# Kernel optimization log

Measured on AMD Instinct MI355X. Metric: run time of the kernel, lower is better.

The kernel has to match this reference:

```python
import jax, jax.numpy as jnp
import numpy as np

B, N, C, O = 1, 8192, 256, 64


def setup_inputs() -> dict:
    key = jax.random.key(0)
    ks = jax.random.split(key, 7)
    return {
        "x": jax.random.normal(ks[0], (B, N, C), dtype=jnp.float32),
        "W1": jax.random.normal(ks[1], (O, C), dtype=jnp.float32) * 0.05,
        "b1": jax.random.normal(ks[2], (O,), dtype=jnp.float32) * 0.05,
        "a1": jax.random.normal(ks[3], (O,), dtype=jnp.float32) * 0.05,
        "ba1": jax.random.normal(ks[4], (1,), dtype=jnp.float32) * 0.05,
        "a2": jax.random.normal(ks[5], (O,), dtype=jnp.float32) * 0.05,
        "ba2": jax.random.normal(ks[6], (1,), dtype=jnp.float32) * 0.05,
    }


def reference(x, W1, b1, a1, ba1, a2, ba2):
    # conv1 (1x1 Conv1d) == per-node linear: seq_fts [B, O, N]
    seq_fts = jnp.einsum('bnc,oc->bon', x, W1) + b1[None, :, None]
    # conv2_1 / conv2_2 (O -> 1, 1x1): f1, f2 [B, N]
    f1 = jnp.einsum('bon,o->bn', seq_fts, a1) + ba1
    f2 = jnp.einsum('bon,o->bn', seq_fts, a2) + ba2
    # logits[b,i,j] = f1[b,i] + f2[b,j]  -> [B, N, N]
    logits = jax.nn.leaky_relu(f1[:, :, None] + f2[:, None, :], negative_slope=0.01)
    # NOTE: original uses nn.Softmax(dim=1) on [B, N, N] -> normalize over axis 1
    coefs = jax.nn.softmax(logits, axis=1)
    # ret[b,i,o] = sum_j coefs[b,i,j] * seq_fts[b,o,j]  -> [B, N, O]
    ret = jnp.einsum('bij,boj->bio', coefs, seq_fts)
    return jax.nn.elu(ret)
```

## Files before the change

### kernel.cpp

```cpp
#include <hip/hip_runtime.h>
#include <math.h>

#define NN 8192
#define CC 256
#define OO 64
#define JW 8

__global__ __launch_bounds__(256) void k_gemm(
    const float* __restrict__ x, const float* __restrict__ W1,
    const float* __restrict__ b1, const float* __restrict__ a1,
    const float* __restrict__ ba1, const float* __restrict__ a2,
    const float* __restrict__ ba2,
    float* __restrict__ seq,
    float* __restrict__ f1, float* __restrict__ f2,
    float* __restrict__ E1, float* __restrict__ E1s,
    float* __restrict__ eF2, float* __restrict__ eF2s,
    unsigned long long* __restrict__ keys )
{
  __shared__ float w_lds[64][66];
  __shared__ float x_lds[8][256];
  const int t = threadIdx.x;
  const int p = t & 31;
  const int row = t >> 5;
  const int r = blockIdx.x*8 + row;
  for (int q = t; q < 512; q += 256) {
    const int rr = q >> 6, c4 = q & 63;
    ((float4*)x_lds[rr])[c4] = ((const float4*)(x + (size_t)(blockIdx.x*8 + rr)*CC))[c4];
  }
  float c0 = 0.f, c1 = 0.f;
  for (int ct = 0; ct < 4; ++ct) {
    __syncthreads();
    for (int idx = t; idx < 4096; idx += 256) {
      const int o = idx >> 6, cc = idx & 63;
      w_lds[cc][o] = W1[o*CC + ct*64 + cc];
    }
    __syncthreads();
    const float* xr = &x_lds[row][ct*64];
#pragma unroll 4
    for (int c = 0; c < 64; c += 4) {
      const float4 xa = *(const float4*)(xr + c);
      const float2 w0 = *(const float2*)&w_lds[c+0][2*p];
      const float2 w1 = *(const float2*)&w_lds[c+1][2*p];
      const float2 w2 = *(const float2*)&w_lds[c+2][2*p];
      const float2 w3 = *(const float2*)&w_lds[c+3][2*p];
      c0 = fmaf(xa.x, w0.x, c0); c0 = fmaf(xa.y, w1.x, c0);
      c0 = fmaf(xa.z, w2.x, c0); c0 = fmaf(xa.w, w3.x, c0);
      c1 = fmaf(xa.x, w0.y, c1); c1 = fmaf(xa.y, w1.y, c1);
      c1 = fmaf(xa.z, w2.y, c1); c1 = fmaf(xa.w, w3.y, c1);
    }
  }
  const float2 B2 = *(const float2*)&b1[2*p];
  const float v0 = c0 + B2.x, v1 = c1 + B2.y;
  *(float2*)&seq[(size_t)r*OO + 2*p] = make_float2(v0, v1);
  const float2 A1 = *(const float2*)&a1[2*p];
  const float2 A2 = *(const float2*)&a2[2*p];
  float p1 = v0*A1.x + v1*A1.y;
  float p2 = v0*A2.x + v1*A2.y;
#pragma unroll
  for (int d = 1; d < 32; d <<= 1) {
    p1 += __shfl_xor(p1, d, 64);
    p2 += __shfl_xor(p2, d, 64);
  }
  if (p == 0) {
    const float t1 = p1 + ba1[0], t2 = p2 + ba2[0];
    f1[r] = t1; E1[r] = expf(t1); E1s[r] = expf(0.01f*t1);
    f2[r] = t2; eF2[r] = expf(t2); eF2s[r] = expf(0.01f*t2);
    unsigned u;
    u = __float_as_uint(t1); u = (u & 0x80000000u) ? ~u : (u | 0x80000000u);
    keys[r] = ((unsigned long long)u << 32) | (unsigned)r;
    u = __float_as_uint(t2); u = (u & 0x80000000u) ? ~u : (u | 0x80000000u);
    keys[NN + r] = ((unsigned long long)u << 32) | (unsigned)r;
  }
}

__global__ __launch_bounds__(512) void k_rank(
    const unsigned long long* __restrict__ keys,
    const float* __restrict__ f1, const float* __restrict__ E1,
    const float* __restrict__ E1s, const float* __restrict__ f2,
    const float* __restrict__ eF2, const float* __restrict__ eF2s,
    float* __restrict__ s1, float* __restrict__ se1, float* __restrict__ se1s,
    int* __restrict__ inv1,
    float* __restrict__ f2s, float* __restrict__ eF2srt,
    float* __restrict__ eF2ssrt, int* __restrict__ inv)
{
  __shared__ unsigned long long skl[NN];
  const int t = threadIdx.x;
  const int lane = t & 63, wv = t >> 6;
  const int b = blockIdx.x;
  const int arr = b >> 7;
  const int jbw = (b & 127)*64 + wv*JW;
  const unsigned long long* kb = keys + ((size_t)arr << 13);
  for (int q = t; q < NN/2; q += 512)
    ((ulonglong2*)skl)[q] = ((const ulonglong2*)kb)[q];
  __syncthreads();
  unsigned long long K[JW];
#pragma unroll
  for (int q = 0; q < JW; ++q) {
    const unsigned long long kk = skl[jbw + q];
    const unsigned lo = __builtin_amdgcn_readfirstlane((unsigned)kk);
    const unsigned hi = __builtin_amdgcn_readfirstlane((unsigned)(kk >> 32));
    K[q] = ((unsigned long long)hi << 32) | lo;
  }
  int cnt[JW];
#pragma unroll
  for (int q = 0; q < JW; ++q) cnt[q] = 0;
  const ulonglong2* s2 = (const ulonglong2*)skl;
#pragma unroll 2
  for (int c = 0; c < NN/128; ++c) {
    const ulonglong2 sk = s2[c*64 + lane];
#pragma unroll
    for (int q = 0; q < JW; ++q) {
      cnt[q] += (sk.x < K[q]) ? 1 : 0;
      cnt[q] += (sk.y < K[q]) ? 1 : 0;
    }
  }
#pragma unroll
  for (int q = 0; q < JW; ++q) {
    int r = cnt[q];
#pragma unroll
    for (int d = 1; d < 64; d <<= 1) r += __shfl_xor(r, d, 64);
    if (lane == 0) {
      const int i = jbw + q;
      if (arr == 0) {
        s1[r] = f1[i]; se1[r] = E1[i]; se1s[r] = E1s[i]; inv1[r] = i;
      } else {
        inv[r] = i; f2s[r] = f2[i]; eF2srt[r] = eF2[i]; eF2ssrt[r] = eF2s[i];
      }
    }
  }
}

__global__ __launch_bounds__(1024) void k_DT(
    const float* __restrict__ se1, const float* __restrict__ se1s,
    const float* __restrict__ s1g,
    const float* __restrict__ f2s, const float* __restrict__ eF2srt,
    const float* __restrict__ eF2ssrt, const int* __restrict__ inv,
    const float* __restrict__ seq,
    float* __restrict__ Bs, float* __restrict__ Es,
    int* __restrict__ kpos, float* __restrict__ TU, float* __restrict__ TV)
{
  __shared__ float s1l[NN];
  __shared__ float f2sl[NN];
  __shared__ float csA[256], csB[256];
  __shared__ float csEA[257], csEB[257];
  __shared__ float wsA[4], wsB[4];
  __shared__ float bsl[32], esl[32];
  __shared__ float redU[16][64], redV[16][64];
  const int t = threadIdx.x;
  const int b = blockIdx.x;
  const int wv = t >> 6, lane = t & 63;
  const float4 a0 = ((const float4*)se1 )[t*2];
  const float4 a1v = ((const float4*)se1 )[t*2+1];
  const float4 b0 = ((const float4*)se1s)[t*2];
  const float4 b1v = ((const float4*)se1s)[t*2+1];
  ((float4*)s1l)[t*2]   = ((const float4*)s1g)[t*2];
  ((float4*)s1l)[t*2+1] = ((const float4*)s1g)[t*2+1];
  ((float4*)f2sl)[t*2]   = ((const float4*)f2s)[t*2];
  ((float4*)f2sl)[t*2+1] = ((const float4*)f2s)[t*2+1];
  float sa = ((a0.x+a0.y)+(a0.z+a0.w)) + ((a1v.x+a1v.y)+(a1v.z+a1v.w));
  float sb = ((b0.x+b0.y)+(b0.z+b0.w)) + ((b1v.x+b1v.y)+(b1v.z+b1v.w));
  sa += __shfl_xor(sa, 1, 64); sb += __shfl_xor(sb, 1, 64);
  sa += __shfl_xor(sa, 2, 64); sb += __shfl_xor(sb, 2, 64);
  if ((t & 3) == 0) { csA[t>>2] = sa; csB[t>>2] = sb; }
  __syncthreads();
  if (t < 256) {
    float a = csA[t], bv = csB[t];
#pragma unroll
    for (int d = 1; d < 64; d <<= 1) {
      const float ua = __shfl_up(a, d, 64);
      const float ub = __shfl_up(bv, d, 64);
      if (lane >= d) { a += ua; bv += ub; }
    }
    csA[t] = a; csB[t] = bv;
    if (lane == 63) { wsA[wv] = a; wsB[wv] = bv; }
  }
  __syncthreads();
  if (t < 256) {
    float baseA = 0.f, baseB = 0.f;
    for (int q = 0; q < wv; ++q) { baseA += wsA[q]; baseB += wsB[q]; }
    csEA[t+1] = csA[t] + baseA;
    csEB[t+1] = csB[t] + baseB;
    if (t == 0) { csEA[0] = 0.f; csEB[0] = 0.f; }
  }
  __syncthreads();
  const int half = lane >> 5, m = lane & 31;
  {
    const int kk = b*32 + 2*wv + half;
    const float tgt = -f2sl[kk];
    int pos = 0;
#pragma unroll
    for (int s = NN; s; s >>= 1) {
      const int c = pos + s;
      if (c <= NN && s1l[c-1] < tgt) pos = c;
    }
    const int base = pos & ~31, cn = pos & 31;
    float ta = 0.f, tb = 0.f;
    if (m < cn) { ta = se1[base+m]; tb = se1s[base+m]; }
#pragma unroll
    for (int d = 1; d < 32; d <<= 1) {
      ta += __shfl_xor(ta, d, 64);
      tb += __shfl_xor(tb, d, 64);
    }
    if (m == 0) {
      const float PreA = csEA[pos>>5] + ta;
      const float PreB = csEB[pos>>5] + tb;
      const float T1 = csEA[256];
      const float e2 = eF2srt[kk], e2s = eF2ssrt[kk];
      const float D = fmaf(T1 - PreA, e2, PreB * e2s);
      const float bsv = e2 / D, esv = e2s / D;
      Bs[kk] = bsv; Es[kk] = esv;
      bsl[2*wv + half] = bsv; esl[2*wv + half] = esv;
    }
  }
  if (t < 32) {
    const int r = b*32 + t;
    const float tgt = -s1l[r];
    int pos = 0;
#pragma unroll
    for (int s = NN; s; s >>= 1) {
      const int c = pos + s;
      if (c <= NN && f2sl[c-1] < tgt) pos = c;
    }
    kpos[r] = pos;
  }
  __syncthreads();
  {
    const int kk0 = b*32 + 2*wv, kk1 = kk0 + 1;
    const float s0v = seq[(size_t)inv[kk0]*OO + lane];
    const float s1v = seq[(size_t)inv[kk1]*OO + lane];
    redU[wv][lane] = bsl[2*wv]*s0v + bsl[2*wv+1]*s1v;
    redV[wv][lane] = esl[2*wv]*s0v + esl[2*wv+1]*s1v;
  }
  __syncthreads();
  if (wv == 0) {
    float r = 0.f;
#pragma unroll
    for (int q = 0; q < 16; ++q) r += redU[q][lane];
    TU[b*64 + lane] = r;
  } else if (wv == 1) {
    float r = 0.f;
#pragma unroll
    for (int q = 0; q < 16; ++q) r += redV[q][lane];
    TV[b*64 + lane] = r;
  }
}

__global__ __launch_bounds__(1024) void k_merge(
    const int* __restrict__ kpos, const int* __restrict__ inv,
    const int* __restrict__ inv1,
    const float* __restrict__ se1, const float* __restrict__ se1s,
    const float* __restrict__ Bs, const float* __restrict__ Es,
    const float* __restrict__ seq,
    const float* __restrict__ TU, const float* __restrict__ TV,
    float* __restrict__ out)
{
  __shared__ int kposl[NN];
  __shared__ float pu[33][64], pv[33][64];
  __shared__ float rA[16][64], rB[16][64], rC[16][64];
  __shared__ int bnd[2];
  const int t = threadIdx.x, lane = t & 63, wv = t >> 6, b = blockIdx.x;
  for (int q = t; q < NN/4; q += 1024)
    ((int4*)kposl)[q] = ((const int4*)kpos)[q];
  float pbu = 0.f, pbv = 0.f, ptu = 0.f;
  for (int c = wv; c < 256; c += 16) {
    const float tu = TU[c*64 + lane], tv = TV[c*64 + lane];
    ptu += tu;
    if (c < b) { pbu += tu; pbv += tv; }
  }
  rA[wv][lane] = pbu; rB[wv][lane] = pbv; rC[wv][lane] = ptu;
  {
    const int kk0 = b*32 + 2*wv, kk1 = kk0 + 1;
    const float sv0 = seq[(size_t)inv[kk0]*OO + lane];
    const float sv1 = seq[(size_t)inv[kk1]*OO + lane];
    pu[2*wv+1][lane] = Bs[kk0]*sv0; pv[2*wv+1][lane] = Es[kk0]*sv0;
    pu[2*wv+2][lane] = Bs[kk1]*sv1; pv[2*wv+2][lane] = Es[kk1]*sv1;
  }
  if (wv == 0) { pu[0][lane] = 0.f; pv[0][lane] = 0.f; }
  __syncthreads();
  if (t == 0) {
    const int hi = 32*b + 32 + (b == 255 ? 1 : 0);
    int pos = 0;
    for (int s = NN; s; s >>= 1) { const int c = pos+s; if (c <= NN && kposl[c-1] >= hi) pos = c; }
    bnd[0] = pos;
    pos = 0;
    const int lo = 32*b;
    for (int s = NN; s; s >>= 1) { const int c = pos+s; if (c <= NN && kposl[c-1] >= lo) pos = c; }
    bnd[1] = pos;
  }
  float base_u = 0.f, base_v = 0.f, utot = 0.f;
#pragma unroll
  for (int q = 0; q < 16; ++q) {
    base_u += rA[q][lane]; base_v += rB[q][lane]; utot += rC[q][lane];
  }
  for (int d = 1; d < 32; d <<= 1) {
    const int rowA = wv + 1;
    const int rowB = wv + 17;
    const int srcA = rowA - d, srcB = rowB - d;
    const float aA = (srcA >= 0) ? pu[srcA][lane] : 0.f;
    const float vA = (srcA >= 0) ? pv[srcA][lane] : 0.f;
    const float aB = (srcB >= 0) ? pu[srcB][lane] : 0.f;
    const float vB = (srcB >= 0) ? pv[srcB][lane] : 0.f;
    __syncthreads();
    pu[rowA][lane] += aA; pv[rowA][lane] += vA;
    pu[rowB][lane] += aB; pv[rowB][lane] += vB;
    __syncthreads();
  }
  const int r0 = bnd[0], r1 = bnd[1];
  for (int r = r0 + wv; r < r1; r += 16) {
    const int kl = kposl[r] - 32*b;
    const float ret = se1[r]*(utot - (base_u + pu[kl][lane]))
                    + se1s[r]*(base_v + pv[kl][lane]);
    out[(size_t)inv1[r]*OO + lane] = (ret > 0.f) ? ret : expm1f(ret);
  }
}

extern "C" void kernel_launch(void* const* d_in, const int* in_sizes, int n_in,
                              void* d_out, int out_size, void* d_ws, size_t ws_size,
                              hipStream_t stream)
{
  (void)in_sizes; (void)n_in; (void)out_size; (void)ws_size;
  const float* x   = (const float*)d_in[0];
  const float* W1  = (const float*)d_in[1];
  const float* b1  = (const float*)d_in[2];
  const float* a1  = (const float*)d_in[3];
  const float* ba1 = (const float*)d_in[4];
  const float* a2  = (const float*)d_in[5];
  const float* ba2 = (const float*)d_in[6];
  float* out = (float*)d_out;

  float* w = (float*)d_ws;
  size_t off = 0;
  auto alloc = [&](size_t n) { float* p = w + off; off += (n + 63) & ~(size_t)63; return p; };
  float* seq  = alloc((size_t)NN*OO);
  float* f1   = alloc(NN);
  float* f2   = alloc(NN);
  float* E1   = alloc(NN);
  float* E1s  = alloc(NN);
  float* eF2  = alloc(NN);
  float* eF2s = alloc(NN);
  unsigned long long* keys = (unsigned long long*)alloc((size_t)4*NN);
  int*   inv1 = (int*)alloc(NN);
  int*   inv  = (int*)alloc(NN);
  float* s1   = alloc(NN);
  float* se1  = alloc(NN);
  float* se1s = alloc(NN);
  float* f2s  = alloc(NN);
  float* eF2srt  = alloc(NN);
  float* eF2ssrt = alloc(NN);
  float* Bs   = alloc(NN);
  float* Es   = alloc(NN);
  int*   kpos = (int*)alloc(NN);
  float* TU   = alloc(256*64);
  float* TV   = alloc(256*64);

  k_gemm<<<1024, 256, 0, stream>>>(x, W1, b1, a1, ba1, a2, ba2,
                                   seq, f1, f2, E1, E1s, eF2, eF2s, keys);
  k_rank<<<256, 512, 0, stream>>>(keys, f1, E1, E1s, f2, eF2, eF2s,
                                  s1, se1, se1s, inv1, f2s, eF2srt, eF2ssrt, inv);
  k_DT<<<256, 1024, 0, stream>>>(se1, se1s, s1, f2s, eF2srt, eF2ssrt,
                                 inv, seq, Bs, Es, kpos, TU, TV);
  k_merge<<<256, 1024, 0, stream>>>(kpos, inv, inv1, se1, se1s, Bs, Es,
                                    seq, TU, TV, out);
}
```

Before: 54.78 us.

## Compute x·W1 projection with split-bf16 MFMA instead of FP32 FMAs

Rewrites the first GEMM kernel to split x and W1 into bf16 high/low parts and accumulate three MFMA 16x16x32 products, which approximates FP32 accuracy. Each block now handles 16 rows, with one wave per 16 output columns, and W1 is read directly from global memory instead of being staged in LDS. f1/f2 are reduced from an LDS copy of the output tile. This targets the scalar FMA cost of the projection but adds split overhead and drops the low×low term, which costs a little precision.

```diff
diff --git a/kernel.cpp b/kernel.cpp
--- a/kernel.cpp
+++ b/kernel.cpp
@@ -5,6 +5,18 @@
 #define CC 256
 #define OO 64
 #define JW 8
+
+using short8 = __attribute__((ext_vector_type(8))) short;
+using f32x4  = __attribute__((ext_vector_type(4))) float;
+
+__device__ __forceinline__ void split2(const float a, const float b,
+                                       unsigned& hp, unsigned& lp) {
+  const unsigned ua = __float_as_uint(a), ub = __float_as_uint(b);
+  hp = (ua >> 16) | (ub & 0xffff0000u);
+  const float la = a - __uint_as_float(ua & 0xffff0000u);
+  const float lb = b - __uint_as_float(ub & 0xffff0000u);
+  lp = (__float_as_uint(la) >> 16) | (__float_as_uint(lb) & 0xffff0000u);
+}
 
 __global__ __launch_bounds__(256) void k_gemm(
     const float* __restrict__ x, const float* __restrict__ W1,
@@ -17,59 +29,87 @@
     float* __restrict__ eF2, float* __restrict__ eF2s,
     unsigned long long* __restrict__ keys )
 {
-  __shared__ float w_lds[64][66];
-  __shared__ float x_lds[8][256];
+  __shared__ unsigned short xh[16][264];
+  __shared__ unsigned short xl[16][264];
+  __shared__ float seq_l[16][66];
   const int t = threadIdx.x;
-  const int p = t & 31;
-  const int row = t >> 5;
-  const int r = blockIdx.x*8 + row;
-  for (int q = t; q < 512; q += 256) {
-    const int rr = q >> 6, c4 = q & 63;
-    ((float4*)x_lds[rr])[c4] = ((const float4*)(x + (size_t)(blockIdx.x*8 + rr)*CC))[c4];
-  }
-  float c0 = 0.f, c1 = 0.f;
-  for (int ct = 0; ct < 4; ++ct) {
-    __syncthreads();
-    for (int idx = t; idx < 4096; idx += 256) {
-      const int o = idx >> 6, cc = idx & 63;
-      w_lds[cc][o] = W1[o*CC + ct*64 + cc];
-    }
-    __syncthreads();
-    const float* xr = &x_lds[row][ct*64];
-#pragma unroll 4
-    for (int c = 0; c < 64; c += 4) {
-      const float4 xa = *(const float4*)(xr + c);
-      const float2 w0 = *(const float2*)&w_lds[c+0][2*p];
-      const float2 w1 = *(const float2*)&w_lds[c+1][2*p];
-      const float2 w2 = *(const float2*)&w_lds[c+2][2*p];
-      const float2 w3 = *(const float2*)&w_lds[c+3][2*p];
-      c0 = fmaf(xa.x, w0.x, c0); c0 = fmaf(xa.y, w1.x, c0);
-      c0 = fmaf(xa.z, w2.x, c0); c0 = fmaf(xa.w, w3.x, c0);
-      c1 = fmaf(xa.x, w0.y, c1); c1 = fmaf(xa.y, w1.y, c1);
-      c1 = fmaf(xa.z, w2.y, c1); c1 = fmaf(xa.w, w3.y, c1);
-    }
-  }
-  const float2 B2 = *(const float2*)&b1[2*p];
-  const float v0 = c0 + B2.x, v1 = c1 + B2.y;
-  *(float2*)&seq[(size_t)r*OO + 2*p] = make_float2(v0, v1);
-  const float2 A1 = *(const float2*)&a1[2*p];
-  const float2 A2 = *(const float2*)&a2[2*p];
-  float p1 = v0*A1.x + v1*A1.y;
-  float p2 = v0*A2.x + v1*A2.y;
-#pragma unroll
-  for (int d = 1; d < 32; d <<= 1) {
-    p1 += __shfl_xor(p1, d, 64);
-    p2 += __shfl_xor(p2, d, 64);
-  }
-  if (p == 0) {
-    const float t1 = p1 + ba1[0], t2 = p2 + ba2[0];
-    f1[r] = t1; E1[r] = expf(t1); E1s[r] = expf(0.01f*t1);
-    f2[r] = t2; eF2[r] = expf(t2); eF2s[r] = expf(0.01f*t2);
-    unsigned u;
-    u = __float_as_uint(t1); u = (u & 0x80000000u) ? ~u : (u | 0x80000000u);
-    keys[r] = ((unsigned long long)u << 32) | (unsigned)r;
-    u = __float_as_uint(t2); u = (u & 0x80000000u) ? ~u : (u | 0x80000000u);
-    keys[NN + r] = ((unsigned long long)u << 32) | (unsigned)r;
+  const int lane = t & 63, wv = t >> 6;
+  const int r0 = blockIdx.x * 16;
+  for (int q = t; q < 1024; q += 256) {
+    const int row = q >> 6, c4 = (q & 63) * 4;
+    const float4 v = *(const float4*)(x + (size_t)(r0 + row)*CC + c4);
+    unsigned hp0, lp0, hp1, lp1;
+    split2(v.x, v.y, hp0, lp0);
+    split2(v.z, v.w, hp1, lp1);
+    const int di = (row*264 + c4) >> 1;
+    ((unsigned*)xh)[di]   = hp0; ((unsigned*)xh)[di+1] = hp1;
+    ((unsigned*)xl)[di]   = lp0; ((unsigned*)xl)[di+1] = lp1;
+  }
+  __syncthreads();
+  const int lr = lane & 15;
+  const int ls = lane >> 4;
+  const int o0 = wv * 16;
+  const float* wrow = W1 + (size_t)(o0 + lr)*CC;
+  const unsigned short* xhr = &xh[lr][0];
+  const unsigned short* xlr = &xl[lr][0];
+  f32x4 acc = {0.f, 0.f, 0.f, 0.f};
+#pragma unroll
+  for (int kc = 0; kc < CC; kc += 32) {
+    const int ko = kc + ls*8;
+    const short8 a_hi = *(const short8*)(xhr + ko);
+    const short8 a_lo = *(const short8*)(xlr + ko);
+    const float4 w0 = *(const float4*)(wrow + ko);
+    const float4 w1 = *(const float4*)(wrow + ko + 4);
+    unsigned bh0, bl0, bh1, bl1, bh2, bl2, bh3, bl3;
+    split2(w0.x, w0.y, bh0, bl0);
+    split2(w0.z, w0.w, bh1, bl1);
+    split2(w1.x, w1.y, bh2, bl2);
+    split2(w1.z, w1.w, bh3, bl3);
+    short8 b_hi, b_lo;
+    b_hi[0] = (short)(bh0 & 0xffff); b_hi[1] = (short)(bh0 >> 16);
+    b_hi[2] = (short)(bh1 & 0xffff); b_hi[3] = (short)(bh1 >> 16);
+    b_hi[4] = (short)(bh2 & 0xffff); b_hi[5] = (short)(bh2 >> 16);
+    b_hi[6] = (short)(bh3 & 0xffff); b_hi[7] = (short)(bh3 >> 16);
+    b_lo[0] = (short)(bl0 & 0xffff); b_lo[1] = (short)(bl0 >> 16);
+    b_lo[2] = (short)(bl1 & 0xffff); b_lo[3] = (short)(bl1 >> 16);
+    b_lo[4] = (short)(bl2 & 0xffff); b_lo[5] = (short)(bl2 >> 16);
+    b_lo[6] = (short)(bl3 & 0xffff); b_lo[7] = (short)(bl3 >> 16);
+    acc = __builtin_amdgcn_mfma_f32_16x16x32_bf16(a_hi, b_hi, acc, 0, 0, 0);
+    acc = __builtin_amdgcn_mfma_f32_16x16x32_bf16(a_lo, b_hi, acc, 0, 0, 0);
+    acc = __builtin_amdgcn_mfma_f32_16x16x32_bf16(a_hi, b_lo, acc, 0, 0, 0);
+  }
+  const int col_g = o0 + lr;
+  const float bb = b1[col_g];
+#pragma unroll
+  for (int j = 0; j < 4; ++j) {
+    const int rowt = 4*ls + j;
+    const float val = acc[j] + bb;
+    seq[(size_t)(r0 + rowt)*OO + col_g] = val;
+    seq_l[rowt][col_g] = val;
+  }
+  __syncthreads();
+  const float A1 = a1[lane], A2 = a2[lane];
+#pragma unroll
+  for (int rr = 0; rr < 4; ++rr) {
+    const int row = 4*wv + rr;
+    const float v = seq_l[row][lane];
+    float p1 = v*A1, p2 = v*A2;
+#pragma unroll
+    for (int d = 1; d < 64; d <<= 1) {
+      p1 += __shfl_xor(p1, d, 64);
+      p2 += __shfl_xor(p2, d, 64);
+    }
+    if (lane == 0) {
+      const int i = r0 + row;
+      const float t1 = p1 + ba1[0], t2 = p2 + ba2[0];
+      f1[i] = t1; E1[i] = expf(t1); E1s[i] = expf(0.01f*t1);
+      f2[i] = t2; eF2[i] = expf(t2); eF2s[i] = expf(0.01f*t2);
+      unsigned u;
+      u = __float_as_uint(t1); u = (u & 0x80000000u) ? ~u : (u | 0x80000000u);
+      keys[i] = ((unsigned long long)u << 32) | (unsigned)i;
+      u = __float_as_uint(t2); u = (u & 0x80000000u) ? ~u : (u | 0x80000000u);
+      keys[NN + i] = ((unsigned long long)u << 32) | (unsigned)i;
+    }
   }
 }
 
@@ -353,8 +393,8 @@
   float* TU   = alloc(256*64);
   float* TV   = alloc(256*64);
 
-  k_gemm<<<1024, 256, 0, stream>>>(x, W1, b1, a1, ba1, a2, ba2,
-                                   seq, f1, f2, E1, E1s, eF2, eF2s, keys);
+  k_gemm<<<512, 256, 0, stream>>>(x, W1, b1, a1, ba1, a2, ba2,
+                                  seq, f1, f2, E1, E1s, eF2, eF2s, keys);
   k_rank<<<256, 512, 0, stream>>>(keys, f1, E1, E1s, f2, eF2, eF2s,
                                   s1, se1, se1s, inv1, f2s, eF2srt, eF2ssrt, inv);
   k_DT<<<256, 1024, 0, stream>>>(se1, se1s, s1, f2s, eF2srt, eF2ssrt,
```

New measurement: 47.03 us. -14.1%, faster.
